# Kernel tuning notes

Measured on AMD Instinct MI355X. Metric: run time of the kernel, lower is better.

## Reference

```python
import jax, jax.numpy as jnp
import numpy as np

# Fixed production-scale dims (equal-size graphs -> no ragged padding needed)
B, NPG, C, H, L, FFN, NC = 16, 512, 128, 8, 4, 512, 4
D = C // H          # head dim = 16
T = NPG + 1         # +1 virtual graph token
EPG = 8192          # edges per graph (avg degree 16)
E = B * EPG


def _ln(x, g, b, eps=1e-5):
    m = x.mean(-1, keepdims=True)
    v = ((x - m) ** 2).mean(-1, keepdims=True)
    return (x - m) * jax.lax.rsqrt(v + eps) * g + b


def setup_inputs() -> dict:
    key = jax.random.key(0)
    ks = jax.random.split(key, 24)
    N = B * NPG
    node_feats = jax.random.normal(ks[0], (N, 3), jnp.float32)
    # intra-graph edges: local endpoints + per-graph node offset (matches batch_ptr math)
    local = jax.random.randint(ks[1], (2, B, EPG), 0, NPG)
    offs = (jnp.arange(B) * NPG)[None, :, None]
    edge_index = (local + offs).reshape(2, E)
    edge_attr = jax.random.randint(ks[2], (E,), 0, 10)

    def nrm(k, shape, scale=0.02):
        return jax.random.normal(k, shape, jnp.float32) * scale

    params = {
        "W_node": nrm(ks[3], (3, C), 0.3), "b_node": jnp.zeros((C,), jnp.float32),
        "graph_token": nrm(ks[4], (C,), 1.0),
        "edge_bias_table": nrm(ks[5], (11, H), 0.1).at[0].set(0.0),  # padding_idx=0
        "in_deg_emb": nrm(ks[6], (512, C)).at[0].set(0.0),           # padding_idx=0
        "out_deg_emb": nrm(ks[7], (512, C)).at[0].set(0.0),
        "vnode_bias": nrm(ks[8], (H,), 1.0),
        "Wq": nrm(ks[9], (L, C, C)), "bq": jnp.zeros((L, C), jnp.float32),
        "Wk": nrm(ks[10], (L, C, C)), "bk": jnp.zeros((L, C), jnp.float32),
        "Wv": nrm(ks[11], (L, C, C)), "bv": jnp.zeros((L, C), jnp.float32),
        "Wo": nrm(ks[12], (L, C, C)), "bo": jnp.zeros((L, C), jnp.float32),
        "ln1_g": jnp.ones((L, C), jnp.float32), "ln1_b": jnp.zeros((L, C), jnp.float32),
        "ln2_g": jnp.ones((L, C), jnp.float32), "ln2_b": jnp.zeros((L, C), jnp.float32),
        "W1": nrm(ks[13], (L, C, FFN)), "b1": jnp.zeros((L, FFN), jnp.float32),
        "W2": nrm(ks[14], (L, FFN, C)), "b2": jnp.zeros((L, C), jnp.float32),
        "normf_g": jnp.ones((C,), jnp.float32), "normf_b": jnp.zeros((C,), jnp.float32),
        "Wc1": nrm(ks[15], (C, C // 2)), "bc1": jnp.zeros((C // 2,), jnp.float32),
        "Wc2": nrm(ks[16], (C // 2, NC)), "bc2": jnp.zeros((NC,), jnp.float32),
    }
    return {"node_feats": node_feats, "edge_index": edge_index,
            "edge_attr": edge_attr, "num_graphs": B, **params}


def reference(node_feats, W_node, b_node, graph_token, edge_bias_table,
              in_deg_emb, out_deg_emb, vnode_bias,
              Wq, bq, Wk, bk, Wv, bv, Wo, bo,
              ln1_g, ln1_b, ln2_g, ln2_b, W1, b1, W2, b2,
              normf_g, normf_b, Wc1, bc1, Wc2, bc2,
              edge_index, edge_attr, num_graphs):
    N = node_feats.shape[0]
    npg = N // num_graphs
    t = npg + 1
    src, dst = edge_index[0], edge_index[1]
    # degree encoders (scatter_add of ones == segment_sum)
    in_deg = jnp.clip(jax.ops.segment_sum(jnp.ones_like(dst), dst, num_segments=N), 0, 511)
    out_deg = jnp.clip(jax.ops.segment_sum(jnp.ones_like(src), src, num_segments=N), 0, 511)
    x_enc = node_feats @ W_node + b_node + in_deg_emb[in_deg] + out_deg_emb[out_deg]
    # equal-size graphs with sorted batch ids -> padding loop is a reshape, mask all-False
    x = jnp.concatenate(
        [jnp.broadcast_to(graph_token, (num_graphs, 1, C)),
         x_enc.reshape(num_graphs, npg, C)], axis=1)  # [B, T, C]
    # attention bias: vnode row/col + scattered edge-attr embeddings
    bias = jnp.zeros((num_graphs, H, t, t), jnp.float32)
    bias = bias.at[:, :, 0, :].set(vnode_bias[None, :, None])
    bias = bias.at[:, :, :, 0].set(vnode_bias[None, :, None])
    eb = edge_bias_table[jnp.clip(edge_attr, 0, 9) + 1]  # [E, H]
    g = src // npg
    sl = src - g * npg + 1
    dl = dst - g * npg + 1
    bias = bias.at[g, :, sl, dl].add(eb)  # duplicate edges accumulate (scatter_add)
    scale = 1.0 / np.sqrt(D).astype(np.float32)
    for l in range(L):  # key_padding_mask is all-False here -> masked_fill is a no-op
        h = _ln(x, ln1_g[l], ln1_b[l])
        q = (h @ Wq[l] + bq[l]).reshape(num_graphs, t, H, D)
        k = (h @ Wk[l] + bk[l]).reshape(num_graphs, t, H, D)
        v = (h @ Wv[l] + bv[l]).reshape(num_graphs, t, H, D)
        scores = jnp.einsum('bthd,bshd->bhts', q, k) * scale + bias
        attn = jax.nn.softmax(scores, axis=-1)
        o = jnp.einsum('bhts,bshd->bthd', attn, v).reshape(num_graphs, t, C)
        x = x + o @ Wo[l] + bo[l]
        h2 = _ln(x, ln2_g[l], ln2_b[l])
        x = x + jax.nn.gelu(h2 @ W1[l] + b1[l], approximate=False) @ W2[l] + b2[l]
    x = _ln(x, normf_g, normf_b)
    gr = x[:, 0, :]  # virtual-node readout
    return jax.nn.gelu(gr @ Wc1 + bc1, approximate=False) @ Wc2 + bc2
```

## Files before the change

kernel.cpp:

```cpp
#include <hip/hip_runtime.h>
#include <hip/hip_bf16.h>

#define BB 16
#define NPG 512
#define CC 128
#define HH 8
#define LL 4
#define FFN 512
#define NCLS 4
#define DD 16
#define TT 513
#define EE 131072
#define NNODES 8192
#define ROWS (BB * TT)
#define ECAP 64
#define SP 544
#define SSTR 548

static constexpr size_t XROWS = (size_t)BB * TT;
static constexpr size_t XSZ   = XROWS * CC;
static constexpr size_t VTSZ  = (size_t)BB * HH * DD * SP;

typedef unsigned short ushort_t;
typedef __attribute__((ext_vector_type(8))) short short8;
typedef __attribute__((ext_vector_type(4))) float floatx4;

__device__ __forceinline__ float gelu_exact(float v) {
    return 0.5f * v * (1.0f + erff(v * 0.70710678118654752440f));
}
__device__ __forceinline__ ushort_t f2bf(float f) {
    union { float f; unsigned u; } c; c.f = f;
    unsigned u = c.u;
    return (ushort_t)((u + 0x7FFFu + ((u >> 16) & 1u)) >> 16);
}
__device__ __forceinline__ int swz(int row, int col, int stride) {
    int kb = col >> 3;
    return row * stride + (((kb ^ (row & 7)) << 3) | (col & 7));
}

__device__ __forceinline__ void qkv_stage8(const ushort_t* hs,
                                           const ushort_t* Wtq, const float* bq_,
                                           const ushort_t* Wtk, const float* bk_,
                                           const ushort_t* Wtv, const float* bv_,
                                           ushort_t* qb, ushort_t* kb, ushort_t* vt,
                                           int b, int t0, int wave, int lq, int quad) {
    const short* hsS = (const short*)hs;
    int c = wave * 16 + lq;
    const short* Ws[3] = {(const short*)Wtq, (const short*)Wtk, (const short*)Wtv};
    const float* bs[3] = {bq_, bk_, bv_};
    size_t rB = (size_t)c * CC;

    #pragma unroll
    for (int m = 0; m < 3; ++m) {
        const short* W = Ws[m];
        floatx4 a0 = {0.f,0.f,0.f,0.f};
        #pragma unroll
        for (int k0 = 0; k0 < CC; k0 += 32) {
            short8 af = *(const short8*)(hsS + swz(lq, k0 + quad * 8, 128));
            short8 b0 = *(const short8*)(W + rB + k0 + quad * 8);
            a0 = __builtin_amdgcn_mfma_f32_16x16x32_bf16(af, b0, a0, 0, 0, 0);
        }
        float bv0 = bs[m][c];
        #pragma unroll
        for (int rg = 0; rg < 4; ++rg) {
            int t = t0 + quad * 4 + rg;
            if (t >= TT) continue;
            size_t r = (size_t)b * TT + t;
            float v0 = a0[rg] + bv0;
            if (m == 0) {
                qb[r * CC + c] = f2bf(v0 * 0.25f);
            } else if (m == 1) {
                kb[r * CC + c] = f2bf(v0);
            } else {
                vt[((size_t)(b * HH + wave) * DD + lq) * SP + t] = f2bf(v0);
            }
        }
    }
}

__global__ __launch_bounds__(256) void deg_csr_tr_kernel(const int* __restrict__ ei,
                                                         const int* __restrict__ ea,
                                                         int* __restrict__ deg_in,
                                                         int* __restrict__ deg_out,
                                                         int* __restrict__ cnt,
                                                         int* __restrict__ ebuf,
                                                         const float* __restrict__ Wq,
                                                         const float* __restrict__ Wk,
                                                         const float* __restrict__ Wv,
                                                         const float* __restrict__ Wo,
                                                         const float* __restrict__ W1,
                                                         const float* __restrict__ W2,
                                                         ushort_t* __restrict__ wtqkvo,
                                                         ushort_t* __restrict__ wt1,
                                                         ushort_t* __restrict__ wt2) {
    int bid = blockIdx.x;
    int tid = threadIdx.x;
    if (bid < 512) {
        int e = bid * 256 + tid;
        int src = ei[e], dst = ei[EE + e];
        atomicAdd(&deg_out[src], 1);
        atomicAdd(&deg_in[dst], 1);
        int g = src >> 9;
        int sl = src - (g << 9) + 1;
        int dl = dst - (g << 9) + 1;
        int a = ea[e];
        a = (a < 0) ? 0 : (a > 9 ? 9 : a);
        a += 1;
        int row = g * TT + sl;
        int pos = atomicAdd(&cnt[row], 1);
        if (pos < ECAP) ebuf[(size_t)row * ECAP + pos] = dl | (a << 16);
        return;
    }
    int z = bid - 512;
    const float* src; ushort_t* dst; int K, N, tile;
    if (z < 64) {
        int zz = z >> 2; tile = z & 3;
        int k = zz >> 2, l = zz & 3;
        const float* s4[4] = {Wq, Wk, Wv, Wo};
        src = s4[k] + (size_t)l * CC * CC;
        dst = wtqkvo + (size_t)(k * 4 + l) * 16384;
        K = CC; N = CC;
    } else if (z < 128) {
        int l = (z - 64) >> 4; tile = (z - 64) & 15;
        src = W1 + (size_t)l * CC * FFN;
        dst = wt1 + (size_t)l * 65536;
        K = CC; N = FFN;
    } else {
        int l = (z - 128) >> 4; tile = (z - 128) & 15;
        src = W2 + (size_t)l * FFN * CC;
        dst = wt2 + (size_t)l * 65536;
        K = FFN; N = CC;
    }
    int tilesN = N >> 6;
    int k0 = (tile / tilesN) << 6;
    int n0 = (tile - (tile / tilesN) * tilesN) << 6;
    __shared__ float t[64][65];
    int c = tid & 63, rb = tid >> 6;
    #pragma unroll
    for (int kk = 0; kk < 64; kk += 4)
        t[kk + rb][c] = src[(size_t)(k0 + kk + rb) * N + n0 + c];
    __syncthreads();
    #pragma unroll
    for (int nn = 0; nn < 64; nn += 4)
        dst[(size_t)(n0 + nn + rb) * K + k0 + c] = f2bf(t[c][nn + rb]);
}

__global__ __launch_bounds__(512) void pre_kernel(const float* __restrict__ nf,
                                                  const float* __restrict__ Wn,
                                                  const float* __restrict__ bn,
                                                  const float* __restrict__ gt,
                                                  const float* __restrict__ ide,
                                                  const float* __restrict__ ode,
                                                  const int* __restrict__ deg_in,
                                                  const int* __restrict__ deg_out,
                                                  const float* __restrict__ ln1g_,
                                                  const float* __restrict__ ln1b_,
                                                  const ushort_t* __restrict__ wtqkvo,
                                                  const float* __restrict__ bq_,
                                                  const float* __restrict__ bk_,
                                                  const float* __restrict__ bv_,
                                                  float* __restrict__ x_,
                                                  ushort_t* __restrict__ qb,
                                                  ushort_t* __restrict__ kb,
                                                  ushort_t* __restrict__ vt) {
    int bid = blockIdx.x;
    int tid = threadIdx.x;
    int b = bid / 33, qt = bid - b * 33;
    int t0 = qt * 16;
    int wave = tid >> 6, lane = tid & 63, lq = lane & 15, quad = lane >> 4;

    __shared__ ushort_t hs[16 * 128];
    __shared__ float sred[8][16][2];

    int c = wave * 16 + lq;
    float w0[4];
    #pragma unroll
    for (int rg = 0; rg < 4; ++rg) {
        int t = t0 + quad * 4 + rg;
        int tc = min(t, TT - 1);
        float v0;
        if (tc == 0) {
            v0 = gt[c];
        } else {
            int i = b * NPG + tc - 1;
            float f0 = nf[i*3+0], f1 = nf[i*3+1], f2 = nf[i*3+2];
            v0 = bn[c] + f0*Wn[0*CC + c] + f1*Wn[1*CC + c] + f2*Wn[2*CC + c];
            int di = min(deg_in[i], 511);
            int dq = min(deg_out[i], 511);
            v0 += ide[(size_t)di * CC + c] + ode[(size_t)dq * CC + c];
        }
        if (t < TT) x_[((size_t)b * TT + t) * CC + c] = v0;
        w0[rg] = v0;
    }
    #pragma unroll
    for (int rg = 0; rg < 4; ++rg) {
        float s1 = w0[rg];
        float s2 = w0[rg] * w0[rg];
        #pragma unroll
        for (int m = 1; m < 16; m <<= 1) {
            s1 += __shfl_xor(s1, m, 64);
            s2 += __shfl_xor(s2, m, 64);
        }
        if (lq == 0) { sred[wave][quad*4+rg][0] = s1; sred[wave][quad*4+rg][1] = s2; }
    }
    __syncthreads();
    float g0 = ln1g_[c], lb0 = ln1b_[c];
    #pragma unroll
    for (int rg = 0; rg < 4; ++rg) {
        int row = quad * 4 + rg;
        float S1 = 0.f, S2 = 0.f;
        #pragma unroll
        for (int w = 0; w < 8; ++w) { S1 += sred[w][row][0]; S2 += sred[w][row][1]; }
        float mn = S1 * (1.0f/CC);
        float var = S2 * (1.0f/CC) - mn * mn;
        float rs = rsqrtf(var + 1e-5f);
        hs[swz(row, c, 128)] = f2bf((w0[rg] - mn) * rs * g0 + lb0);
    }
    __syncthreads();
    qkv_stage8(hs, wtqkvo, bq_,
               wtqkvo + (size_t)4 * 16384, bk_,
               wtqkvo + (size_t)8 * 16384, bv_,
               qb, kb, vt, b, t0, wave, lq, quad);
}

__global__ __launch_bounds__(256, 4) void attn_kernel(const ushort_t* __restrict__ qbr,
                                                      const ushort_t* __restrict__ kbr,
                                                      const ushort_t* __restrict__ vtr,
                                                      const int* __restrict__ cnt,
                                                      const int* __restrict__ ebuf,
                                                      const float* __restrict__ ebt,
                                                      const float* __restrict__ vnode,
                                                      ushort_t* __restrict__ obf) {
    int qt = blockIdx.x;
    int bh = blockIdx.y;
    int b = bh >> 3, h = bh & (HH - 1);
    int tid = threadIdx.x;
    int wave = tid >> 6, lane = tid & 63, lq = lane & 15, quad = lane >> 4;

    __shared__ __align__(16) float strip[16 * SSTR];
    __shared__ __align__(16) int elist[16 * 64];
    __shared__ float ebtl[12];
    __shared__ int cn_s[16];

    for (int i = tid; i < 16 * SSTR / 4; i += 256)
        ((float4*)strip)[i] = make_float4(0.f, 0.f, 0.f, 0.f);
    if (tid < 11) ebtl[tid] = ebt[tid * 8 + h];
    {
        int r = tid >> 4, j4 = (tid & 15) * 4;
        int qrow = qt * 16 + r;
        bool rv = (qrow >= 1) && (qrow < TT);
        size_t crow = (size_t)b * TT + (rv ? qrow : 0);
        *(int4*)&elist[r * 64 + j4] = *(const int4*)(ebuf + crow * ECAP + j4);
        if ((tid & 15) == 0) cn_s[r] = rv ? min(cnt[crow], ECAP) : 0;
    }
    __syncthreads();
    if (tid < 16) {
        int qrow = qt * 16 + tid;
        if (qrow >= 1 && qrow < TT) strip[tid * SSTR] = vnode[h];
    }
    {
        int r = tid >> 4;
        int cn = cn_s[r];
        for (int j = tid & 15; j < cn; j += 16) {
            int e = elist[r * 64 + j];
            atomicAdd(&strip[r * SSTR + (e & 0xFFFF)], ebtl[e >> 16]);
        }
    }
    __syncthreads();

    int qg = qt * 16 + lq;
    int qr = min(qg, TT - 1);
    short8 z8 = {0,0,0,0,0,0,0,0};
    short8 qf = z8;
    if (quad < 2)
        qf = *(const short8*)(qbr + ((size_t)(b * TT + qr)) * CC + h * DD + quad * 8);
    const short* kbS = (const short*)kbr;
    const short* vtS = (const short*)(vtr + (size_t)bh * DD * SP);

    floatx4 oacc = {0.f, 0.f, 0.f, 0.f};
    float lsum = 0.f;

    short8 af0c = z8, af1c = z8, vfc;
    {
        int sp = wave;
        int st0 = sp * 2, st1 = st0 + 1;
        int kr0 = min(b * TT + st0 * 16 + lq, (int)XROWS - 1);
        int kr1 = min(b * TT + st1 * 16 + lq, (int)XROWS - 1);
        if (quad < 2) {
            af0c = *(const short8*)(kbS + (size_t)kr0 * CC + h * DD + quad * 8);
            af1c = *(const short8*)(kbS + (size_t)kr1 * CC + h * DD + quad * 8);
        }
        vfc = *(const short8*)(vtS + (size_t)lq * SP + sp * 32 + quad * 8);
    }

    for (int sp = wave; sp < 17; sp += 4) {
        int spn = sp + 4;
        short8 af0n = z8, af1n = z8, vfn = z8;
        if (spn < 17) {
            int st0 = spn * 2, st1 = st0 + 1;
            int kr0 = min(b * TT + st0 * 16 + lq, (int)XROWS - 1);
            int kr1 = min(b * TT + st1 * 16 + lq, (int)XROWS - 1);
            if (quad < 2) {
                af0n = *(const short8*)(kbS + (size_t)kr0 * CC + h * DD + quad * 8);
                af1n = *(const short8*)(kbS + (size_t)kr1 * CC + h * DD + quad * 8);
            }
            vfn = *(const short8*)(vtS + (size_t)lq * SP + spn * 32 + quad * 8);
        }

        int roff = lq * SSTR + sp * 32 + quad * 4;
        float4 bia = *(const float4*)&strip[roff];
        float4 bib = *(const float4*)&strip[roff + 16];

        unsigned pw[2][2];
        #pragma unroll
        for (int t = 0; t < 2; ++t) {
            int st = sp * 2 + t;
            floatx4 cc4 = __builtin_amdgcn_mfma_f32_16x16x32_bf16(
                t ? af1c : af0c, qf, (floatx4){0.f, 0.f, 0.f, 0.f}, 0, 0, 0);
            float4 bi = t ? bib : bia;
            float biv[4] = {bi.x, bi.y, bi.z, bi.w};
            float pr[4];
            #pragma unroll
            for (int rg = 0; rg < 4; ++rg) {
                int s = st * 16 + quad * 4 + rg;
                float p = 0.f;
                if (s < TT) p = __expf(cc4[rg] + biv[rg]);
                lsum += p;
                pr[rg] = p;
            }
            pw[t][0] = (unsigned)f2bf(pr[0]) | ((unsigned)f2bf(pr[1]) << 16);
            pw[t][1] = (unsigned)f2bf(pr[2]) | ((unsigned)f2bf(pr[3]) << 16);
        }
        int srcA = lq + (((2 * quad) & 3) << 4);
        int srcB = lq + (((2 * quad + 1) & 3) << 4);
        int a00 = __shfl((int)pw[0][0], srcA, 64);
        int a01 = __shfl((int)pw[0][1], srcA, 64);
        int a10 = __shfl((int)pw[1][0], srcA, 64);
        int a11 = __shfl((int)pw[1][1], srcA, 64);
        int b00 = __shfl((int)pw[0][0], srcB, 64);
        int b01 = __shfl((int)pw[0][1], srcB, 64);
        int b10 = __shfl((int)pw[1][0], srcB, 64);
        int b11 = __shfl((int)pw[1][1], srcB, 64);
        union { int u[4]; short8 s8; } pu;
        bool lo = quad < 2;
        pu.u[0] = lo ? a00 : a10;
        pu.u[1] = lo ? a01 : a11;
        pu.u[2] = lo ? b00 : b10;
        pu.u[3] = lo ? b01 : b11;
        oacc = __builtin_amdgcn_mfma_f32_16x16x32_bf16(vfc, pu.s8, oacc, 0, 0, 0);

        af0c = af0n; af1c = af1n; vfc = vfn;
    }

    lsum += __shfl_xor(lsum, 16, 64);
    lsum += __shfl_xor(lsum, 32, 64);
    __syncthreads();
    float* redw = strip;
    float* lsumS = strip + 1088;
    #pragma unroll
    for (int rg = 0; rg < 4; ++rg)
        redw[wave * 272 + (quad * 4 + rg) * 17 + lq] = oacc[rg];
    if (quad == 0) lsumS[wave * 16 + lq] = lsum;
    __syncthreads();
    {
        int q = tid >> 4, d = tid & 15;
        float o = 0.f, L = 0.f;
        #pragma unroll
        for (int w = 0; w < 4; ++w) {
            o += redw[w * 272 + d * 17 + q];
            L += lsumS[w * 16 + q];
        }
        int qq = qt * 16 + q;
        if (qq < TT)
            obf[((size_t)(b * TT + qq)) * CC + h * DD + d] = f2bf(o / L);
    }
}

__global__ __launch_bounds__(512, 4) void mega_kernel(const ushort_t* __restrict__ obf,
                                                      const ushort_t* __restrict__ WtO,
                                                      const float* __restrict__ bo_,
                                                      const float* __restrict__ ln2g_,
                                                      const float* __restrict__ ln2b_,
                                                      const ushort_t* __restrict__ Wt1_,
                                                      const float* __restrict__ b1_,
                                                      const ushort_t* __restrict__ Wt2_,
                                                      const float* __restrict__ b2_,
                                                      const float* __restrict__ ln1g_,
                                                      const float* __restrict__ ln1b_,
                                                      const ushort_t* __restrict__ Wtq,
                                                      const float* __restrict__ bq_,
                                                      const ushort_t* __restrict__ Wtk,
                                                      const float* __restrict__ bk_,
                                                      const ushort_t* __restrict__ Wtv,
                                                      const float* __restrict__ bv_,
                                                      const float* __restrict__ nfg,
                                                      const float* __restrict__ nfb,
                                                      const float* __restrict__ Wc1,
                                                      const float* __restrict__ bc1,
                                                      const float* __restrict__ Wc2,
                                                      const float* __restrict__ bc2,
                                                      float* __restrict__ x_,
                                                      ushort_t* __restrict__ qbw,
                                                      ushort_t* __restrict__ kbw,
                                                      ushort_t* __restrict__ vtw,
                                                      float* __restrict__ out,
                                                      int doQKV) {
    int qt = blockIdx.x, b = blockIdx.y;
    int tid = threadIdx.x;
    int wave = tid >> 6, lane = tid & 63, lq = lane & 15, quad = lane >> 4;

    __shared__ __align__(16) ushort_t hs[16 * 128];
    __shared__ __align__(16) ushort_t ms[16 * 512];
    __shared__ float sred[8][16][2];

    int t0 = qt * 16;
    int c = wave * 16 + lq;
    float vv0[4];

    {
        const short* obS = (const short*)obf;
        size_t arow = (size_t)b * TT + min(t0 + lq, TT - 1);
        const short* W = (const short*)WtO;
        size_t rB = (size_t)c * CC;
        floatx4 a0 = {0.f,0.f,0.f,0.f};
        #pragma unroll
        for (int k0 = 0; k0 < CC; k0 += 32) {
            short8 af = *(const short8*)(obS + arow * CC + k0 + quad * 8);
            short8 b0 = *(const short8*)(W + rB + k0 + quad * 8);
            a0 = __builtin_amdgcn_mfma_f32_16x16x32_bf16(af, b0, a0, 0, 0, 0);
        }
        float bv0 = bo_[c];
        #pragma unroll
        for (int rg = 0; rg < 4; ++rg) {
            int t = t0 + quad * 4 + rg;
            size_t rc = (size_t)b * TT + min(t, TT - 1);
            vv0[rg] = a0[rg] + bv0 + x_[rc * CC + c];
        }
        #pragma unroll
        for (int rg = 0; rg < 4; ++rg) {
            float s1 = vv0[rg];
            float s2 = vv0[rg] * vv0[rg];
            #pragma unroll
            for (int m = 1; m < 16; m <<= 1) {
                s1 += __shfl_xor(s1, m, 64);
                s2 += __shfl_xor(s2, m, 64);
            }
            if (lq == 0) { sred[wave][quad*4+rg][0] = s1; sred[wave][quad*4+rg][1] = s2; }
        }
        __syncthreads();
        float g0 = ln2g_[c], lb0 = ln2b_[c];
        #pragma unroll
        for (int rg = 0; rg < 4; ++rg) {
            int row = quad * 4 + rg;
            float S1 = 0.f, S2 = 0.f;
            #pragma unroll
            for (int w = 0; w < 8; ++w) { S1 += sred[w][row][0]; S2 += sred[w][row][1]; }
            float mn = S1 * (1.0f/CC);
            float var = S2 * (1.0f/CC) - mn * mn;
            float rs = rsqrtf(var + 1e-5f);
            hs[swz(row, c, 128)] = f2bf((vv0[rg] - mn) * rs * g0 + lb0);
        }
    }
    __syncthreads();

    {
        const short* hsS = (const short*)hs;
        const short* W = (const short*)Wt1_;
        #pragma unroll
        for (int nt = 0; nt < 4; ++nt) {
            int n = wave * 64 + nt * 16;
            size_t rB = (size_t)(n + lq) * CC;
            floatx4 a0 = {0.f,0.f,0.f,0.f};
            #pragma unroll
            for (int k0 = 0; k0 < CC; k0 += 32) {
                short8 af = *(const short8*)(hsS + swz(lq, k0 + quad * 8, 128));
                short8 b0 = *(const short8*)(W + rB + k0 + quad * 8);
                a0 = __builtin_amdgcn_mfma_f32_16x16x32_bf16(af, b0, a0, 0, 0, 0);
            }
            float bb0 = b1_[n + lq];
            #pragma unroll
            for (int rg = 0; rg < 4; ++rg)
                ms[swz(quad * 4 + rg, n + lq, 512)] = f2bf(gelu_exact(a0[rg] + bb0));
        }
    }
    __syncthreads();

    float w0[4];
    {
        const short* msS = (const short*)ms;
        const short* W = (const short*)Wt2_;
        size_t rB = (size_t)c * FFN;
        floatx4 a0 = {0.f,0.f,0.f,0.f};
        #pragma unroll 8
        for (int k0 = 0; k0 < FFN; k0 += 32) {
            short8 af = *(const short8*)(msS + swz(lq, k0 + quad * 8, 512));
            short8 b0 = *(const short8*)(W + rB + k0 + quad * 8);
            a0 = __builtin_amdgcn_mfma_f32_16x16x32_bf16(af, b0, a0, 0, 0, 0);
        }
        float bv0 = b2_[c];
        #pragma unroll
        for (int rg = 0; rg < 4; ++rg) {
            int t = t0 + quad * 4 + rg;
            w0[rg] = a0[rg] + bv0 + vv0[rg];
            if (t < TT) x_[((size_t)b * TT + t) * CC + c] = w0[rg];
        }
    }

    if (doQKV) {
        #pragma unroll
        for (int rg = 0; rg < 4; ++rg) {
            float s1 = w0[rg];
            float s2 = w0[rg] * w0[rg];
            #pragma unroll
            for (int m = 1; m < 16; m <<= 1) {
                s1 += __shfl_xor(s1, m, 64);
                s2 += __shfl_xor(s2, m, 64);
            }
            if (lq == 0) { sred[wave][quad*4+rg][0] = s1; sred[wave][quad*4+rg][1] = s2; }
        }
        __syncthreads();
        float g0 = ln1g_[c], lb0 = ln1b_[c];
        #pragma unroll
        for (int rg = 0; rg < 4; ++rg) {
            int row = quad * 4 + rg;
            float S1 = 0.f, S2 = 0.f;
            #pragma unroll
            for (int w = 0; w < 8; ++w) { S1 += sred[w][row][0]; S2 += sred[w][row][1]; }
            float mn = S1 * (1.0f/CC);
            float var = S2 * (1.0f/CC) - mn * mn;
            float rs = rsqrtf(var + 1e-5f);
            hs[swz(row, c, 128)] = f2bf((w0[rg] - mn) * rs * g0 + lb0);
        }
        __syncthreads();
        qkv_stage8(hs, Wtq, bq_, Wtk, bk_, Wtv, bv_, qbw, kbw, vtw, b, t0, wave, lq, quad);
        return;
    }

    if (qt != 0) return;

    __syncthreads();
    float* hrow = (float*)ms;
    float* xfs  = hrow + CC;
    float* c1s  = xfs + CC;
    float* red  = c1s + 64;
    if (quad == 0) hrow[c] = w0[0];
    __syncthreads();

    {
        int ct = tid;
        float v = 0.f, s1 = 0.f, s2 = 0.f;
        if (ct < CC) { v = hrow[ct]; s1 = v; s2 = v * v; }
        #pragma unroll
        for (int m = 32; m >= 1; m >>= 1) {
            s1 += __shfl_xor(s1, m, 64);
            s2 += __shfl_xor(s2, m, 64);
        }
        int w = ct >> 6;
        if (ct < CC && (ct & 63) == 0) { red[w*2] = s1; red[w*2+1] = s2; }
        __syncthreads();
        if (ct < CC) {
            float S1 = red[0] + red[2], S2 = red[1] + red[3];
            float mn = S1 * (1.0f/CC);
            float var = S2 * (1.0f/CC) - mn * mn;
            float rs = rsqrtf(var + 1e-5f);
            xfs[ct] = (v - mn) * rs * nfg[ct] + nfb[ct];
        }
        __syncthreads();
        if (ct < 64) {
            float acc = bc1[ct];
            #pragma unroll 4
            for (int k = 0; k < CC; ++k) acc = fmaf(xfs[k], Wc1[(size_t)k * 64 + ct], acc);
            c1s[ct] = gelu_exact(acc);
        }
        __syncthreads();
        if (ct < NCLS) {
            float acc = bc2[ct];
            #pragma unroll 4
            for (int j = 0; j < 64; ++j) acc = fmaf(c1s[j], Wc2[(size_t)j * NCLS + ct], acc);
            out[(size_t)b * NCLS + ct] = acc;
        }
    }
}

extern "C" void kernel_launch(void* const* d_in, const int* in_sizes, int n_in,
                              void* d_out, int out_size, void* d_ws, size_t ws_size,
                              hipStream_t stream) {
    const float* node_feats = (const float*)d_in[0];
    const int*   edge_index = (const int*)d_in[1];
    const int*   edge_attr  = (const int*)d_in[2];
    const float* W_node  = (const float*)d_in[4];
    const float* b_node  = (const float*)d_in[5];
    const float* g_token = (const float*)d_in[6];
    const float* ebt     = (const float*)d_in[7];
    const float* ide     = (const float*)d_in[8];
    const float* ode     = (const float*)d_in[9];
    const float* vnode   = (const float*)d_in[10];
    const float* Wq = (const float*)d_in[11];
    const float* bq = (const float*)d_in[12];
    const float* Wk = (const float*)d_in[13];
    const float* bk = (const float*)d_in[14];
    const float* Wv = (const float*)d_in[15];
    const float* bv = (const float*)d_in[16];
    const float* Wo = (const float*)d_in[17];
    const float* bo = (const float*)d_in[18];
    const float* ln1g = (const float*)d_in[19];
    const float* ln1b = (const float*)d_in[20];
    const float* ln2g = (const float*)d_in[21];
    const float* ln2b = (const float*)d_in[22];
    const float* W1 = (const float*)d_in[23];
    const float* b1 = (const float*)d_in[24];
    const float* W2 = (const float*)d_in[25];
    const float* b2 = (const float*)d_in[26];
    const float* nfg = (const float*)d_in[27];
    const float* nfb = (const float*)d_in[28];
    const float* Wc1 = (const float*)d_in[29];
    const float* bc1 = (const float*)d_in[30];
    const float* Wc2 = (const float*)d_in[31];
    const float* bc2 = (const float*)d_in[32];
    float* out = (float*)d_out;

    char* base = (char*)d_ws;
    float* x      = (float*)base;     base += XSZ * 4;
    ushort_t* qb0 = (ushort_t*)base;  base += XSZ * 2;
    ushort_t* kb0 = (ushort_t*)base;  base += XSZ * 2;
    ushort_t* vt0 = (ushort_t*)base;  base += VTSZ * 2;
    ushort_t* qb1 = (ushort_t*)base;  base += XSZ * 2;
    ushort_t* kb1 = (ushort_t*)base;  base += XSZ * 2;
    ushort_t* vt1 = (ushort_t*)base;  base += VTSZ * 2;
    ushort_t* obf = (ushort_t*)base;  base += XSZ * 2;
    ushort_t* wtqkvo = (ushort_t*)base; base += (size_t)16 * 16384 * 2;
    ushort_t* wt1 = (ushort_t*)base;  base += (size_t)4 * 65536 * 2;
    ushort_t* wt2 = (ushort_t*)base;  base += (size_t)4 * 65536 * 2;
    int* deg_in  = (int*)base;        base += NNODES * 4;
    int* deg_out = (int*)base;        base += NNODES * 4;
    int* cnt     = (int*)base;        base += (size_t)ROWS * 4;
    int* ebuf    = (int*)base;        base += (size_t)ROWS * ECAP * 4;

    ushort_t* qbs[2] = {qb0, qb1};
    ushort_t* kbs[2] = {kb0, kb1};
    ushort_t* vts[2] = {vt0, vt1};

    hipMemsetAsync(deg_in, 0, (size_t)(2 * NNODES + ROWS) * 4, stream);
    deg_csr_tr_kernel<<<512 + 192, 256, 0, stream>>>(
        edge_index, edge_attr, deg_in, deg_out, cnt, ebuf,
        Wq, Wk, Wv, Wo, W1, W2, wtqkvo, wt1, wt2);

    pre_kernel<<<528, 512, 0, stream>>>(
        node_feats, W_node, b_node, g_token, ide, ode, deg_in, deg_out,
        ln1g, ln1b, wtqkvo, bq, bk, bv, x, qb0, kb0, vt0);

    for (int l = 0; l < LL; ++l) {
        int rd = l & 1, wr = rd ^ 1;
        int ln = (l + 1) % LL;

        attn_kernel<<<dim3(33, BB * HH), 256, 0, stream>>>(
            qbs[rd], kbs[rd], vts[rd], cnt, ebuf, ebt, vnode, obf);

        mega_kernel<<<dim3(33, BB), 512, 0, stream>>>(
            obf,
            wtqkvo + (size_t)(12 + l)*16384, bo + l*CC,
            ln2g + l*CC, ln2b + l*CC,
            wt1 + (size_t)l*65536, b1 + l*FFN,
            wt2 + (size_t)l*65536, b2 + l*CC,
            ln1g + ln*CC, ln1b + ln*CC,
            wtqkvo + (size_t)(0 + ln)*16384, bq + ln*CC,
            wtqkvo + (size_t)(4 + ln)*16384, bk + ln*CC,
            wtqkvo + (size_t)(8 + ln)*16384, bv + ln*CC,
            nfg, nfb, Wc1, bc1, Wc2, bc2,
            x, qbs[wr], kbs[wr], vts[wr], out,
            (l < LL-1) ? 1 : 0);
    }
}
```

Before: 450.6 us.

## Store Q/K head-major and prefetch residual and FFN weights early in mega kernel

Q and K are now written in a head-major [b,h,t,d] layout, so the attention kernel reads each head's 16-element rows contiguously instead of pulling 32-byte pieces out of 256-byte token rows. The mega kernel also loads the residual x values and the first half of its W1 weight fragments at kernel start, so their latency overlaps the output-projection stage. The Q/K writes in the QKV stage become more scattered, and holding the prefetched fragments adds register pressure.

```diff
diff --git a/kernel.cpp b/kernel.cpp
--- a/kernel.cpp
+++ b/kernel.cpp
@@ -42,7 +42,7 @@
                                            const ushort_t* Wtq, const float* bq_,
                                            const ushort_t* Wtk, const float* bk_,
                                            const ushort_t* Wtv, const float* bv_,
-                                           ushort_t* qb, ushort_t* kb, ushort_t* vt,
+                                           ushort_t* qh, ushort_t* kh, ushort_t* vt,
                                            int b, int t0, int wave, int lq, int quad) {
     const short* hsS = (const short*)hs;
     int c = wave * 16 + lq;
@@ -65,12 +65,12 @@
         for (int rg = 0; rg < 4; ++rg) {
             int t = t0 + quad * 4 + rg;
             if (t >= TT) continue;
-            size_t r = (size_t)b * TT + t;
             float v0 = a0[rg] + bv0;
+            size_t hr = ((size_t)(b * HH + wave) * TT + t) * DD + lq;
             if (m == 0) {
-                qb[r * CC + c] = f2bf(v0 * 0.25f);
+                qh[hr] = f2bf(v0 * 0.25f);
             } else if (m == 1) {
-                kb[r * CC + c] = f2bf(v0);
+                kh[hr] = f2bf(v0);
             } else {
                 vt[((size_t)(b * HH + wave) * DD + lq) * SP + t] = f2bf(v0);
             }
@@ -160,8 +160,8 @@
                                                   const float* __restrict__ bk_,
                                                   const float* __restrict__ bv_,
                                                   float* __restrict__ x_,
-                                                  ushort_t* __restrict__ qb,
-                                                  ushort_t* __restrict__ kb,
+                                                  ushort_t* __restrict__ qh,
+                                                  ushort_t* __restrict__ kh,
                                                   ushort_t* __restrict__ vt) {
     int bid = blockIdx.x;
     int tid = threadIdx.x;
@@ -220,11 +220,11 @@
     qkv_stage8(hs, wtqkvo, bq_,
                wtqkvo + (size_t)4 * 16384, bk_,
                wtqkvo + (size_t)8 * 16384, bv_,
-               qb, kb, vt, b, t0, wave, lq, quad);
-}
-
-__global__ __launch_bounds__(256, 4) void attn_kernel(const ushort_t* __restrict__ qbr,
-                                                      const ushort_t* __restrict__ kbr,
+               qh, kh, vt, b, t0, wave, lq, quad);
+}
+
+__global__ __launch_bounds__(256, 4) void attn_kernel(const ushort_t* __restrict__ qhr,
+                                                      const ushort_t* __restrict__ khr,
                                                       const ushort_t* __restrict__ vtr,
                                                       const int* __restrict__ cnt,
                                                       const int* __restrict__ ebuf,
@@ -271,10 +271,11 @@
     int qg = qt * 16 + lq;
     int qr = min(qg, TT - 1);
     short8 z8 = {0,0,0,0,0,0,0,0};
+    const short* qhS = (const short*)qhr;
+    const short* khS = (const short*)khr;
     short8 qf = z8;
     if (quad < 2)
-        qf = *(const short8*)(qbr + ((size_t)(b * TT + qr)) * CC + h * DD + quad * 8);
-    const short* kbS = (const short*)kbr;
+        qf = *(const short8*)(qhS + ((size_t)bh * TT + qr) * DD + quad * 8);
     const short* vtS = (const short*)(vtr + (size_t)bh * DD * SP);
 
     floatx4 oacc = {0.f, 0.f, 0.f, 0.f};
@@ -283,12 +284,11 @@
     short8 af0c = z8, af1c = z8, vfc;
     {
         int sp = wave;
-        int st0 = sp * 2, st1 = st0 + 1;
-        int kr0 = min(b * TT + st0 * 16 + lq, (int)XROWS - 1);
-        int kr1 = min(b * TT + st1 * 16 + lq, (int)XROWS - 1);
+        int t0r = min(sp * 2 * 16 + lq, TT - 1);
+        int t1r = min((sp * 2 + 1) * 16 + lq, TT - 1);
         if (quad < 2) {
-            af0c = *(const short8*)(kbS + (size_t)kr0 * CC + h * DD + quad * 8);
-            af1c = *(const short8*)(kbS + (size_t)kr1 * CC + h * DD + quad * 8);
+            af0c = *(const short8*)(khS + ((size_t)bh * TT + t0r) * DD + quad * 8);
+            af1c = *(const short8*)(khS + ((size_t)bh * TT + t1r) * DD + quad * 8);
         }
         vfc = *(const short8*)(vtS + (size_t)lq * SP + sp * 32 + quad * 8);
     }
@@ -297,12 +297,11 @@
         int spn = sp + 4;
         short8 af0n = z8, af1n = z8, vfn = z8;
         if (spn < 17) {
-            int st0 = spn * 2, st1 = st0 + 1;
-            int kr0 = min(b * TT + st0 * 16 + lq, (int)XROWS - 1);
-            int kr1 = min(b * TT + st1 * 16 + lq, (int)XROWS - 1);
+            int t0r = min(spn * 2 * 16 + lq, TT - 1);
+            int t1r = min((spn * 2 + 1) * 16 + lq, TT - 1);
             if (quad < 2) {
-                af0n = *(const short8*)(kbS + (size_t)kr0 * CC + h * DD + quad * 8);
-                af1n = *(const short8*)(kbS + (size_t)kr1 * CC + h * DD + quad * 8);
+                af0n = *(const short8*)(khS + ((size_t)bh * TT + t0r) * DD + quad * 8);
+                af1n = *(const short8*)(khS + ((size_t)bh * TT + t1r) * DD + quad * 8);
             }
             vfn = *(const short8*)(vtS + (size_t)lq * SP + spn * 32 + quad * 8);
         }
@@ -400,8 +399,8 @@
                                                       const float* __restrict__ Wc2,
                                                       const float* __restrict__ bc2,
                                                       float* __restrict__ x_,
-                                                      ushort_t* __restrict__ qbw,
-                                                      ushort_t* __restrict__ kbw,
+                                                      ushort_t* __restrict__ qhw,
+                                                      ushort_t* __restrict__ khw,
                                                       ushort_t* __restrict__ vtw,
                                                       float* __restrict__ out,
                                                       int doQKV) {
@@ -417,6 +416,21 @@
     int c = wave * 16 + lq;
     float vv0[4];
 
+    float xr[4];
+    #pragma unroll
+    for (int rg = 0; rg < 4; ++rg) {
+        int t = t0 + quad * 4 + rg;
+        xr[rg] = x_[((size_t)b * TT + min(t, TT - 1)) * CC + c];
+    }
+    const short* W1S = (const short*)Wt1_;
+    short8 w2p[8];
+    #pragma unroll
+    for (int nt = 0; nt < 2; ++nt)
+        #pragma unroll
+        for (int kk = 0; kk < 4; ++kk)
+            w2p[nt*4+kk] = *(const short8*)(W1S + (size_t)(wave * 64 + nt * 16 + lq) * CC
+                                            + kk * 32 + quad * 8);
+
     {
         const short* obS = (const short*)obf;
         size_t arow = (size_t)b * TT + min(t0 + lq, TT - 1);
@@ -431,11 +445,8 @@
         }
         float bv0 = bo_[c];
         #pragma unroll
-        for (int rg = 0; rg < 4; ++rg) {
-            int t = t0 + quad * 4 + rg;
-            size_t rc = (size_t)b * TT + min(t, TT - 1);
-            vv0[rg] = a0[rg] + bv0 + x_[rc * CC + c];
-        }
+        for (int rg = 0; rg < 4; ++rg)
+            vv0[rg] = a0[rg] + bv0 + xr[rg];
         #pragma unroll
         for (int rg = 0; rg < 4; ++rg) {
             float s1 = vv0[rg];
@@ -465,16 +476,17 @@
 
     {
         const short* hsS = (const short*)hs;
-        const short* W = (const short*)Wt1_;
         #pragma unroll
         for (int nt = 0; nt < 4; ++nt) {
             int n = wave * 64 + nt * 16;
             size_t rB = (size_t)(n + lq) * CC;
             floatx4 a0 = {0.f,0.f,0.f,0.f};
             #pragma unroll
-            for (int k0 = 0; k0 < CC; k0 += 32) {
+            for (int kk = 0; kk < 4; ++kk) {
+                int k0 = kk * 32;
                 short8 af = *(const short8*)(hsS + swz(lq, k0 + quad * 8, 128));
-                short8 b0 = *(const short8*)(W + rB + k0 + quad * 8);
+                short8 b0 = (nt < 2) ? w2p[nt*4+kk]
+                                     : *(const short8*)(W1S + rB + k0 + quad * 8);
                 a0 = __builtin_amdgcn_mfma_f32_16x16x32_bf16(af, b0, a0, 0, 0, 0);
             }
             float bb0 = b1_[n + lq];
@@ -532,7 +544,7 @@
             hs[swz(row, c, 128)] = f2bf((w0[rg] - mn) * rs * g0 + lb0);
         }
         __syncthreads();
-        qkv_stage8(hs, Wtq, bq_, Wtk, bk_, Wtv, bv_, qbw, kbw, vtw, b, t0, wave, lq, quad);
+        qkv_stage8(hs, Wtq, bq_, Wtk, bk_, Wtv, bv_, qhw, khw, vtw, b, t0, wave, lq, quad);
         return;
     }
 
@@ -621,11 +633,11 @@
 
     char* base = (char*)d_ws;
     float* x      = (float*)base;     base += XSZ * 4;
-    ushort_t* qb0 = (ushort_t*)base;  base += XSZ * 2;
-    ushort_t* kb0 = (ushort_t*)base;  base += XSZ * 2;
+    ushort_t* qh0 = (ushort_t*)base;  base += XSZ * 2;
+    ushort_t* kh0 = (ushort_t*)base;  base += XSZ * 2;
     ushort_t* vt0 = (ushort_t*)base;  base += VTSZ * 2;
-    ushort_t* qb1 = (ushort_t*)base;  base += XSZ * 2;
-    ushort_t* kb1 = (ushort_t*)base;  base += XSZ * 2;
+    ushort_t* qh1 = (ushort_t*)base;  base += XSZ * 2;
+    ushort_t* kh1 = (ushort_t*)base;  base += XSZ * 2;
     ushort_t* vt1 = (ushort_t*)base;  base += VTSZ * 2;
     ushort_t* obf = (ushort_t*)base;  base += XSZ * 2;
     ushort_t* wtqkvo = (ushort_t*)base; base += (size_t)16 * 16384 * 2;
@@ -636,8 +648,8 @@
     int* cnt     = (int*)base;        base += (size_t)ROWS * 4;
     int* ebuf    = (int*)base;        base += (size_t)ROWS * ECAP * 4;
 
-    ushort_t* qbs[2] = {qb0, qb1};
-    ushort_t* kbs[2] = {kb0, kb1};
+    ushort_t* qhs[2] = {qh0, qh1};
+    ushort_t* khs[2] = {kh0, kh1};
     ushort_t* vts[2] = {vt0, vt1};
 
     hipMemsetAsync(deg_in, 0, (size_t)(2 * NNODES + ROWS) * 4, stream);
@@ -647,14 +659,14 @@
 
     pre_kernel<<<528, 512, 0, stream>>>(
         node_feats, W_node, b_node, g_token, ide, ode, deg_in, deg_out,
-        ln1g, ln1b, wtqkvo, bq, bk, bv, x, qb0, kb0, vt0);
+        ln1g, ln1b, wtqkvo, bq, bk, bv, x, qh0, kh0, vt0);
 
     for (int l = 0; l < LL; ++l) {
         int rd = l & 1, wr = rd ^ 1;
         int ln = (l + 1) % LL;
 
         attn_kernel<<<dim3(33, BB * HH), 256, 0, stream>>>(
-            qbs[rd], kbs[rd], vts[rd], cnt, ebuf, ebt, vnode, obf);
+            qhs[rd], khs[rd], vts[rd], cnt, ebuf, ebt, vnode, obf);
 
         mega_kernel<<<dim3(33, BB), 512, 0, stream>>>(
             obf,
@@ -667,7 +679,7 @@
             wtqkvo + (size_t)(4 + ln)*16384, bk + ln*CC,
             wtqkvo + (size_t)(8 + ln)*16384, bv + ln*CC,
             nfg, nfb, Wc1, bc1, Wc2, bc2,
-            x, qbs[wr], kbs[wr], vts[wr], out,
+            x, qhs[wr], khs[wr], vts[wr], out,
             (l < LL-1) ? 1 : 0);
     }
 }
```

Result: no change. 446.9 us (-0.8%).
